# Kernel tuning notes

Hardware: AMD Instinct MI355X
Metric: run time of the kernel (lower is better)

## Reference

```python
import jax, jax.numpy as jnp
import numpy as np

B, N, CIN, H, D, K = 8, 1000, 16, 64, 16, 3  # batch, nodes, in_dim, hidden, embed_dim, cheb_k
XIN = CIN + H  # GRU concat input dim


def setup_inputs() -> dict:
    key = jax.random.key(0)
    ks = jax.random.split(key, 18)
    f = lambda k, s, sc=1.0: jax.random.normal(k, s, dtype=jnp.float32) * sc
    inp = {}
    inp['x1'] = f(ks[0], (B, N, CIN)); inp['x2'] = f(ks[1], (B, N, CIN)); inp['x3'] = f(ks[2], (B, N, CIN))
    inp['state1'] = f(ks[3], (B, N, H)); inp['state2'] = f(ks[4], (B, N, H)); inp['state3'] = f(ks[5], (B, N, H))
    for i, name in enumerate(['support1', 'support2', 'support3']):
        a = jax.random.uniform(ks[6 + i], (N, N), dtype=jnp.float32)
        inp[name] = a / a.sum(-1, keepdims=True)  # row-stochastic graph, keeps Chebyshev stable
    inp['embeddings1'] = f(ks[9], (N, D), 0.1); inp['embeddings2'] = f(ks[10], (N, D), 0.1); inp['embeddings3'] = f(ks[11], (N, D), 0.1)
    inp['mode_embedding'] = f(ks[12], (3, D), 0.5)
    # xavier-normal-ish scales for the hypernet weight pools
    inp['Wg'] = f(ks[13], (D, K * XIN, 2 * H), (2.0 / (K * XIN * 2 * H + D * 2 * H)) ** 0.5)
    inp['Bg'] = f(ks[14], (D, 2 * H), (2.0 / (D + 2 * H)) ** 0.5)
    inp['Wu'] = f(ks[15], (D, K * XIN, H), (2.0 / (K * XIN * H + D * H)) ** 0.5)
    inp['Bu'] = f(ks[16], (D, H), (2.0 / (D + H)) ** 0.5)
    return inp


def _cheb_gcn(x, support, emb, wp, bp):
    # x:[B,N,C], support:[N,N], emb:[N,D], wp:[D,K*C,O], bp:[D,O]
    # Chebyshev recurrence applied directly to features (equivalent to building T_k(support))
    terms = [x, jnp.einsum('nm,bmc->bnc', support, x)]
    for _ in range(2, K):
        terms.append(2.0 * jnp.einsum('nm,bmc->bnc', support, terms[-1]) - terms[-2])
    x_g = jnp.concatenate(terms, axis=-1)  # [B,N,K*C]
    # meta_axis='S': per-node weights = emb @ wp ; fused contraction
    out = jnp.einsum('bni,nd,dio->bno', x_g, emb, wp) + emb @ bp  # [B,N,O]
    return out


def _cell(x, state, support, emb, me, Wg, Bg, Wu, Bu):
    # me:[D] mode embedding scales the shared pools (einsum 'mc,cdf->mcdf' -> pick mode m)
    zr = jax.nn.sigmoid(_cheb_gcn(jnp.concatenate([x, state], -1), support, emb,
                                  me[:, None, None] * Wg, me[:, None] * Bg))
    z, r = jnp.split(zr, 2, axis=-1)
    hc = jnp.tanh(_cheb_gcn(jnp.concatenate([x, z * state], -1), support, emb,
                            me[:, None, None] * Wu, me[:, None] * Bu))
    return r * state + (1.0 - r) * hc


def reference(x1, x2, x3, state1, state2, state3, support1, support2, support3,
              embeddings1, embeddings2, embeddings3, mode_embedding, Wg, Bg, Wu, Bu):
    h1 = _cell(x1, state1, support1, embeddings1, mode_embedding[0], Wg, Bg, Wu, Bu)
    h2 = _cell(x2, state2, support2, embeddings2, mode_embedding[1], Wg, Bg, Wu, Bu)
    h3 = _cell(x3, state3, support3, embeddings3, mode_embedding[2], Wg, Bg, Wu, Bu)
    return (h1, h2, h3)
```

## Files before the change

kernel.cpp:

```cpp
#include <hip/hip_runtime.h>
#include <math.h>


typedef __attribute__((ext_vector_type(8))) short s16x8;
typedef __attribute__((ext_vector_type(4))) float f32x4;
typedef unsigned short u16;
typedef unsigned int u32;
typedef unsigned long long u64;

__device__ __forceinline__ u32 f2bf(float f) {
  union { float f; u32 u; } v; v.f = f;
  return (v.u + 0x7FFFu + ((v.u >> 16) & 1u)) >> 16;
}
__device__ __forceinline__ float bf2f(u16 h) {
  union { u32 u; float f; } v; v.u = (u32)h << 16; return v.f;
}
__device__ __forceinline__ void glds16(const u16* g, u16* l) {
  __builtin_amdgcn_global_load_lds(
      (const __attribute__((address_space(1))) void*)g,
      (__attribute__((address_space(3))) void*)l, 16, 0, 0);
}

#define E0 3145728
#define E1 1966080
#define E2 1920000
#define E3 384000
#define E4 384000
#define E5 384000
#define E6 119808

struct PrepArgs {
  const float* x[3]; const float* st[3]; const float* S[3];
  u16 *S16, *Xt, *Ag, *AgU, *T1t, *ZSt, *SZ1t;
};

__global__ void prep(PrepArgs P) {
  long idx = (long)blockIdx.x * 256 + threadIdx.x;
  if (idx < E0) {
    int m = (int)(idx >> 20); int rem = (int)(idx & 1048575);
    int n = rem >> 10, k = rem & 1023;
    float v = (n < 1000 && k < 1000) ? P.S[m][n * 1000 + k] : 0.f;
    P.S16[(size_t)m * 1048576 + rem] = (u16)f2bf(v); return;
  }
  idx -= E0;
  if (idx < E1) {
    int m = (int)(idx / 655360); int rem = (int)(idx % 655360);
    int col = rem >> 10, nn = rem & 1023;
    int b = col / 80, c = col % 80;
    float v = 0.f;
    if (nn < 1000) v = (c < 16) ? P.x[m][(b * 1000 + nn) * 16 + c]
                                : P.st[m][(b * 1000 + nn) * 64 + c - 16];
    P.Xt[(size_t)m * 655360 + rem] = (u16)f2bf(v); return;
  }
  idx -= E1;
  if (idx < E2) {
    int m = (int)(idx / 640000); int rem = (int)(idx % 640000);
    int r = rem / 80, c = rem % 80;
    int n = r >> 3, b = r & 7;
    float v = (c < 16) ? P.x[m][(b * 1000 + n) * 16 + c]
                       : P.st[m][(b * 1000 + n) * 64 + c - 16];
    P.Ag[(size_t)m * 2048000 + (size_t)r * 256 + c] = (u16)f2bf(v); return;
  }
  idx -= E2;
  if (idx < E3) {
    int m = (int)(idx / 128000); int rem = (int)(idx % 128000);
    int r = rem / 16, c = 240 + rem % 16;
    P.Ag[(size_t)m * 2048000 + (size_t)r * 256 + c] = 0; return;
  }
  idx -= E3;
  if (idx < E4) {
    int m = (int)(idx / 128000); int rem = (int)(idx % 128000);
    int r = rem / 16, c = rem % 16;
    int n = r >> 3, b = r & 7;
    P.AgU[(size_t)m * 2048000 + (size_t)r * 256 + c] =
        (u16)f2bf(P.x[m][(b * 1000 + n) * 16 + c]); return;
  }
  idx -= E4;
  if (idx < E5) {
    int m = (int)(idx / 128000); int rem = (int)(idx % 128000);
    int r = rem / 16, c = 240 + rem % 16;
    P.AgU[(size_t)m * 2048000 + (size_t)r * 256 + c] = 0; return;
  }
  idx -= E5;
  if (idx < E6) {
    int m = (int)(idx / 39936); int rem = (int)(idx % 39936);
    if (rem < 15360) { int col = rem / 24, j = rem % 24;
      P.T1t[(size_t)m * 655360 + col * 1024 + 1000 + j] = 0; }
    else if (rem < 27648) { int e = rem - 15360; int col = e / 24, j = e % 24;
      P.ZSt[(size_t)m * 524288 + col * 1024 + 1000 + j] = 0; }
    else { int e = rem - 27648; int col = e / 24, j = e % 24;
      P.SZ1t[(size_t)m * 524288 + col * 1024 + 1000 + j] = 0; }
    return;
  }
}

__global__ void bias_kernel(const float* __restrict__ e0, const float* __restrict__ e1,
                            const float* __restrict__ e2, const float* __restrict__ me,
                            const float* __restrict__ Bp, int O, float* __restrict__ outB) {
  int idx = blockIdx.x * blockDim.x + threadIdx.x;
  int total = 3 * 1000 * O;
  if (idx >= total) return;
  int mode = idx / (1000 * O);
  int rem  = idx % (1000 * O);
  int n = rem / O, o = rem % O;
  const float* emb = (mode == 0) ? e0 : (mode == 1) ? e1 : e2;
  float s = 0.f;
#pragma unroll
  for (int d = 0; d < 16; ++d)
    s += emb[n * 16 + d] * me[mode * 16 + d] * Bp[d * O + o];
  outB[idx] = s;
}

__global__ void packW_kernel(const float* __restrict__ Wg, const float* __restrict__ Wu,
                             u16* __restrict__ BtG, u16* __restrict__ BtU) {
  int idx = blockIdx.x * blockDim.x + threadIdx.x;
  if (idx >= (2048 + 1024) * 256) return;
  if (idx < 2048 * 256) {
    int col = idx >> 8, k = idx & 255;
    int d = col >> 7, o = col & 127;
    BtG[idx] = (k < 240) ? (u16)f2bf(Wg[d * 30720 + k * 128 + o]) : (u16)0;
  } else {
    int i2 = idx - 2048 * 256;
    int col = i2 >> 8, k = i2 & 255;
    int d = col >> 6, o = col & 63;
    BtU[i2] = (k < 240) ? (u16)f2bf(Wu[d * 15360 + k * 64 + o]) : (u16)0;
  }
}

struct ChebArgs2 {
  const u16* S16[3]; const u16* A[3]; const u16* Res[3];
  u16* Yt[3]; u16* AgA[3]; u16* AgX[3];
};

__global__ __launch_bounds__(256, 2) void cheb_v4(ChebArgs2 g, int fdiv, int agbase,
                                                  float alpha, float beta, int flags) {
  const int mode = blockIdx.z;
  const u16* __restrict__ Ab = g.A[mode];
  const u16* __restrict__ Sb = g.S16[mode];

  __shared__ u16 As[64 * 64];
  __shared__ u16 Bs[64 * 64];

  const int t = threadIdx.x;
  const int row0 = blockIdx.y * 64, n0 = blockIdx.x * 64;
  const int lane = t & 63, wid = t >> 6;
  const int l16 = lane & 15, quad = lane >> 4;
  const int wy = (wid >> 1) * 32, wx = (wid & 1) * 32;

  f32x4 acc[2][2];
#pragma unroll
  for (int a = 0; a < 2; ++a)
#pragma unroll
    for (int b = 0; b < 2; ++b) acc[a][b] = (f32x4){0.f, 0.f, 0.f, 0.f};

  for (int k0 = 0; k0 < 1024; k0 += 64) {
#pragma unroll
    for (int p = 0; p < 2; ++p) {
      int idx = p * 256 + t; int row = idx >> 3; int cs = (idx & 7) ^ (row & 7);
      glds16(Ab + (size_t)(row0 + row) * 1024 + k0 + cs * 8, &As[idx * 8]);
    }
#pragma unroll
    for (int p = 0; p < 2; ++p) {
      int idx = p * 256 + t; int row = idx >> 3; int cs = (idx & 7) ^ (row & 7);
      glds16(Sb + (size_t)(n0 + row) * 1024 + k0 + cs * 8, &Bs[idx * 8]);
    }
    __syncthreads();
    s16x8 af[2][2], bf[2][2];
#pragma unroll
    for (int mi = 0; mi < 2; ++mi) {
      int row = wy + mi * 16 + l16;
#pragma unroll
      for (int ks = 0; ks < 2; ++ks) {
        int cl = (ks * 4 + quad) ^ (row & 7);
        af[mi][ks] = *(const s16x8*)&As[row * 64 + cl * 8];
      }
    }
#pragma unroll
    for (int ni = 0; ni < 2; ++ni) {
      int row = wx + ni * 16 + l16;
#pragma unroll
      for (int ks = 0; ks < 2; ++ks) {
        int cl = (ks * 4 + quad) ^ (row & 7);
        bf[ni][ks] = *(const s16x8*)&Bs[row * 64 + cl * 8];
      }
    }
#pragma unroll
    for (int ks = 0; ks < 2; ++ks)
#pragma unroll
      for (int mi = 0; mi < 2; ++mi)
#pragma unroll
        for (int ni = 0; ni < 2; ++ni)
          acc[mi][ni] = __builtin_amdgcn_mfma_f32_16x16x32_bf16(af[mi][ks], bf[ni][ks], acc[mi][ni], 0, 0, 0);
    __syncthreads();
  }

#pragma unroll
  for (int mi = 0; mi < 2; ++mi) {
    int frow0 = row0 + wy + mi * 16 + quad * 4;
    int b = frow0 / fdiv, c0 = frow0 - b * fdiv;
#pragma unroll
    for (int ni = 0; ni < 2; ++ni) {
      int n = n0 + wx + ni * 16 + l16;
      if (n < 1000) {
        u16 pk[4];
#pragma unroll
        for (int r = 0; r < 4; ++r) {
          float v = alpha * acc[mi][ni][r];
          if (flags & 1) v += beta * bf2f(g.Res[mode][(size_t)(frow0 + r) * 1024 + n]);
          u16 h = (u16)f2bf(v);
          pk[r] = h;
          if (flags & 2) g.Yt[mode][(size_t)(frow0 + r) * 1024 + n] = h;
        }
        u64 pv = (u64)pk[0] | ((u64)pk[1] << 16) | ((u64)pk[2] << 32) | ((u64)pk[3] << 48);
        *(u64*)&g.AgA[mode][(size_t)(n * 8 + b) * 256 + agbase + c0] = pv;
        if ((flags & 4) && c0 < 16)
          *(u64*)&g.AgX[mode][(size_t)(n * 8 + b) * 256 + agbase + c0] = pv;
      }
    }
  }
}

struct Meta3Args {
  const u16* Ag;
  const u16* Bt;
  const float* emb[3];
  const float* me;
  const float* Bias;
  const float* state[3];
  u16* ZSt;
  u16* AgU;
  float* Rb;
  float* out;
};

__global__ __launch_bounds__(256, 4) void meta3(Meta3Args A, int is_gate, int O) {
  const int mode = blockIdx.z;
  const int row0 = blockIdx.y * 64;
  const int n0 = row0 >> 3;
  const int oc = blockIdx.x;
  const int ocbase = oc * 64;

  __shared__ u16 Bs[64 * 256];
  __shared__ float ewS[8][17];

  const int t = threadIdx.x;
  if (t < 128) {
    int nl = t >> 4, d = t & 15;
    ewS[nl][d] = A.emb[mode][(n0 + nl) * 16 + d] * A.me[mode * 16 + d];
  }

  const int lane = t & 63, wid = t >> 6;
  const int l16 = lane & 15, quad = lane >> 4;
  const int wy = (wid >> 1) * 32, wx = (wid & 1) * 32;
  const u16* Agm = A.Ag + (size_t)mode * 2048000;

#pragma unroll
  for (int p = 0; p < 8; ++p) {
    int idx = p * 256 + t; int row = idx >> 5; int cs = (idx & 31) ^ (row & 7);
    glds16(Agm + (size_t)(row0 + row) * 256 + cs * 8, &Bs[idx * 8]);
  }
  __syncthreads();

  s16x8 afr[2][8];
#pragma unroll
  for (int mi = 0; mi < 2; ++mi) {
    int row = wy + mi * 16 + l16;
#pragma unroll
    for (int ki = 0; ki < 8; ++ki) {
      int cl = (ki * 4 + quad) ^ (row & 7);
      afr[mi][ki] = *(const s16x8*)&Bs[row * 256 + cl * 8];
    }
  }
  __syncthreads();

  f32x4 outacc[2][2];
#pragma unroll
  for (int a = 0; a < 2; ++a)
#pragma unroll
    for (int b = 0; b < 2; ++b) outacc[a][b] = (f32x4){0.f, 0.f, 0.f, 0.f};

  for (int tl = 0; tl < 16; ++tl) {
    const int brow0 = tl * O + ocbase;
#pragma unroll
    for (int p = 0; p < 8; ++p) {
      int idx = p * 256 + t; int row = idx >> 5; int cs = (idx & 31) ^ (row & 7);
      glds16(A.Bt + (size_t)(brow0 + row) * 256 + cs * 8, &Bs[idx * 8]);
    }
    __syncthreads();

    f32x4 acc[2][2];
#pragma unroll
    for (int a = 0; a < 2; ++a)
#pragma unroll
      for (int b = 0; b < 2; ++b) acc[a][b] = (f32x4){0.f, 0.f, 0.f, 0.f};

#pragma unroll
    for (int ki = 0; ki < 8; ++ki) {
      s16x8 bfr[2];
#pragma unroll
      for (int ni = 0; ni < 2; ++ni) {
        int row = wx + ni * 16 + l16;
        int cl = (ki * 4 + quad) ^ (row & 7);
        bfr[ni] = *(const s16x8*)&Bs[row * 256 + cl * 8];
      }
#pragma unroll
      for (int mi = 0; mi < 2; ++mi)
#pragma unroll
        for (int ni = 0; ni < 2; ++ni)
          acc[mi][ni] = __builtin_amdgcn_mfma_f32_16x16x32_bf16(afr[mi][ki], bfr[ni], acc[mi][ni], 0, 0, 0);
    }

#pragma unroll
    for (int mi = 0; mi < 2; ++mi) {
      int nl = (wy + mi * 16 + quad * 4) >> 3;
      float s = ewS[nl][tl];
#pragma unroll
      for (int ni = 0; ni < 2; ++ni)
#pragma unroll
        for (int r = 0; r < 4; ++r)
          outacc[mi][ni][r] += s * acc[mi][ni][r];
    }
    __syncthreads();
  }

#pragma unroll
  for (int mi = 0; mi < 2; ++mi)
#pragma unroll
    for (int ni = 0; ni < 2; ++ni)
#pragma unroll
      for (int r = 0; r < 4; ++r) {
        int row = row0 + wy + mi * 16 + quad * 4 + r;
        int n = row >> 3, b = row & 7;
        int o = ocbase + wx + ni * 16 + l16;
        float pre = outacc[mi][ni][r] + A.Bias[(size_t)mode * 1000 * O + n * O + o];
        if (is_gate) {
          float sg = 1.f / (1.f + __expf(-pre));
          if (o < 64) {
            float st = A.state[mode][(b * 1000 + n) * 64 + o];
            float zs = sg * st;
            A.ZSt[(size_t)mode * 524288 + (size_t)(b * 64 + o) * 1024 + n] = (u16)f2bf(zs);
            A.AgU[(size_t)mode * 2048000 + (size_t)row * 256 + 16 + o] = (u16)f2bf(zs);
          } else {
            A.Rb[(size_t)mode * 512000 + row * 64 + (o - 64)] = sg;
          }
        } else {
          float hc = tanhf(pre);
          float rr = A.Rb[(size_t)mode * 512000 + row * 64 + o];
          float st = A.state[mode][(b * 1000 + n) * 64 + o];
          A.out[(size_t)mode * 512000 + (b * 1000 + n) * 64 + o] = rr * st + (1.f - rr) * hc;
        }
      }
}

extern "C" void kernel_launch(void* const* d_in, const int* in_sizes, int n_in,
                              void* d_out, int out_size, void* d_ws, size_t ws_size,
                              hipStream_t stream) {
  const float* x[3]   = {(const float*)d_in[0], (const float*)d_in[1], (const float*)d_in[2]};
  const float* st[3]  = {(const float*)d_in[3], (const float*)d_in[4], (const float*)d_in[5]};
  const float* S[3]   = {(const float*)d_in[6], (const float*)d_in[7], (const float*)d_in[8]};
  const float* emb[3] = {(const float*)d_in[9], (const float*)d_in[10], (const float*)d_in[11]};
  const float* me = (const float*)d_in[12];
  const float* Wg = (const float*)d_in[13];
  const float* Bg = (const float*)d_in[14];
  const float* Wu = (const float*)d_in[15];
  const float* Bu = (const float*)d_in[16];
  float* out = (float*)d_out;

  float* BiG = (float*)d_ws;
  float* BiU = BiG + 384000;
  float* Rb  = BiU + 192000;
  u16* S16 = (u16*)(Rb + 1536000);
  u16* Xt  = S16 + 3145728;
  u16* T1t = Xt + 1966080;
  u16* ZSt = T1t + 1966080;
  u16* SZ1t= ZSt + 1572864;
  u16* Ag  = SZ1t + 1572864;
  u16* AgU = Ag + 6144000;
  u16* BtG = AgU + 6144000;
  u16* BtU = BtG + 524288;

  {
    PrepArgs P;
    for (int m = 0; m < 3; ++m) { P.x[m] = x[m]; P.st[m] = st[m]; P.S[m] = S[m]; }
    P.S16 = S16; P.Xt = Xt; P.Ag = Ag; P.AgU = AgU; P.T1t = T1t; P.ZSt = ZSt; P.SZ1t = SZ1t;
    prep<<<32436, 256, 0, stream>>>(P);
  }
  bias_kernel<<<1500, 256, 0, stream>>>(emb[0], emb[1], emb[2], me, Bg, 128, BiG);
  bias_kernel<<<750, 256, 0, stream>>>(emb[0], emb[1], emb[2], me, Bu, 64, BiU);
  packW_kernel<<<3072, 256, 0, stream>>>(Wg, Wu, BtG, BtU);

  {
    ChebArgs2 a;
    for (int m = 0; m < 3; ++m) {
      a.S16[m] = S16 + (size_t)m * 1048576; a.A[m] = Xt + (size_t)m * 655360;
      a.Res[m] = nullptr; a.Yt[m] = T1t + (size_t)m * 655360;
      a.AgA[m] = Ag + (size_t)m * 2048000; a.AgX[m] = AgU + (size_t)m * 2048000;
    }
    cheb_v4<<<dim3(16, 10, 3), 256, 0, stream>>>(a, 80, 80, 1.f, 0.f, 2 | 4);
  }
  {
    ChebArgs2 a;
    for (int m = 0; m < 3; ++m) {
      a.S16[m] = S16 + (size_t)m * 1048576; a.A[m] = T1t + (size_t)m * 655360;
      a.Res[m] = Xt + (size_t)m * 655360; a.Yt[m] = nullptr;
      a.AgA[m] = Ag + (size_t)m * 2048000; a.AgX[m] = AgU + (size_t)m * 2048000;
    }
    cheb_v4<<<dim3(16, 10, 3), 256, 0, stream>>>(a, 80, 160, 2.f, -1.f, 1 | 4);
  }
  {
    Meta3Args a;
    a.Ag = Ag; a.Bt = BtG; a.me = me; a.Bias = BiG;
    a.ZSt = ZSt; a.AgU = AgU; a.Rb = Rb; a.out = out;
    for (int m = 0; m < 3; ++m) { a.emb[m] = emb[m]; a.state[m] = st[m]; }
    meta3<<<dim3(2, 125, 3), 256, 0, stream>>>(a, 1, 128);
  }
  {
    ChebArgs2 a;
    for (int m = 0; m < 3; ++m) {
      a.S16[m] = S16 + (size_t)m * 1048576; a.A[m] = ZSt + (size_t)m * 524288;
      a.Res[m] = nullptr; a.Yt[m] = SZ1t + (size_t)m * 524288;
      a.AgA[m] = AgU + (size_t)m * 2048000; a.AgX[m] = nullptr;
    }
    cheb_v4<<<dim3(16, 8, 3), 256, 0, stream>>>(a, 64, 96, 1.f, 0.f, 2);
  }
  {
    ChebArgs2 a;
    for (int m = 0; m < 3; ++m) {
      a.S16[m] = S16 + (size_t)m * 1048576; a.A[m] = SZ1t + (size_t)m * 524288;
      a.Res[m] = ZSt + (size_t)m * 524288; a.Yt[m] = nullptr;
      a.AgA[m] = AgU + (size_t)m * 2048000; a.AgX[m] = nullptr;
    }
    cheb_v4<<<dim3(16, 8, 3), 256, 0, stream>>>(a, 64, 176, 2.f, -1.f, 1);
  }
  {
    Meta3Args a;
    a.Ag = AgU; a.Bt = BtU; a.me = me; a.Bias = BiU;
    a.ZSt = ZSt; a.AgU = AgU; a.Rb = Rb; a.out = out;
    for (int m = 0; m < 3; ++m) { a.emb[m] = emb[m]; a.state[m] = st[m]; }
    meta3<<<dim3(1, 125, 3), 256, 0, stream>>>(a, 0, 64);
  }
}
```

Measured before the change: 271.7 us.

## Pre-swizzle weight pool into MFMA fragment layout and load B fragments directly

The weight-pool packing now writes bf16 weights in the exact per-lane MFMA B-fragment order, so meta3 can read B fragments straight from global memory into registers with coalesced 16-byte loads. This removes the per-tile LDS staging of B and the two block-wide barriers per tile. The price is more register pressure from holding 16 fragment vectors, so launch bounds drop from 4 to 3 blocks per SM, and every wave now issues its own global loads (likely L2-served) where the block used to share one LDS copy.

New measurement: 280.3 us. 1.03x slower.

```diff
diff --git a/kernel.cpp b/kernel.cpp
--- a/kernel.cpp
+++ b/kernel.cpp
@@ -115,14 +115,18 @@
                              u16* __restrict__ BtG, u16* __restrict__ BtU) {
   int idx = blockIdx.x * blockDim.x + threadIdx.x;
   if (idx >= (2048 + 1024) * 256) return;
-  if (idx < 2048 * 256) {
-    int col = idx >> 8, k = idx & 255;
-    int d = col >> 7, o = col & 127;
+  if (idx < 524288) {
+    int e = idx & 7, lane = (idx >> 3) & 63, ki = (idx >> 9) & 7;
+    int j = (idx >> 12) & 7, d = idx >> 15;
+    int k = ki * 32 + (lane >> 4) * 8 + e;
+    int o = j * 16 + (lane & 15);
     BtG[idx] = (k < 240) ? (u16)f2bf(Wg[d * 30720 + k * 128 + o]) : (u16)0;
   } else {
-    int i2 = idx - 2048 * 256;
-    int col = i2 >> 8, k = i2 & 255;
-    int d = col >> 6, o = col & 63;
+    int i2 = idx - 524288;
+    int e = i2 & 7, lane = (i2 >> 3) & 63, ki = (i2 >> 9) & 7;
+    int j = (i2 >> 12) & 3, d = i2 >> 14;
+    int k = ki * 32 + (lane >> 4) * 8 + e;
+    int o = j * 16 + (lane & 15);
     BtU[i2] = (k < 240) ? (u16)f2bf(Wu[d * 15360 + k * 64 + o]) : (u16)0;
   }
 }
@@ -233,14 +237,15 @@
   float* out;
 };
 
-__global__ __launch_bounds__(256, 4) void meta3(Meta3Args A, int is_gate, int O) {
+__global__ __launch_bounds__(256, 3) void meta3(Meta3Args A, int is_gate, int O) {
   const int mode = blockIdx.z;
   const int row0 = blockIdx.y * 64;
   const int n0 = row0 >> 3;
   const int oc = blockIdx.x;
   const int ocbase = oc * 64;
-
-  __shared__ u16 Bs[64 * 256];
+  const int J = O >> 4;
+
+  __shared__ u16 As[64 * 256];
   __shared__ float ewS[8][17];
 
   const int t = threadIdx.x;
@@ -257,7 +262,7 @@
 #pragma unroll
   for (int p = 0; p < 8; ++p) {
     int idx = p * 256 + t; int row = idx >> 5; int cs = (idx & 31) ^ (row & 7);
-    glds16(Agm + (size_t)(row0 + row) * 256 + cs * 8, &Bs[idx * 8]);
+    glds16(Agm + (size_t)(row0 + row) * 256 + cs * 8, &As[idx * 8]);
   }
   __syncthreads();
 
@@ -268,10 +273,9 @@
 #pragma unroll
     for (int ki = 0; ki < 8; ++ki) {
       int cl = (ki * 4 + quad) ^ (row & 7);
-      afr[mi][ki] = *(const s16x8*)&Bs[row * 256 + cl * 8];
-    }
-  }
-  __syncthreads();
+      afr[mi][ki] = *(const s16x8*)&As[row * 256 + cl * 8];
+    }
+  }
 
   f32x4 outacc[2][2];
 #pragma unroll
@@ -279,14 +283,16 @@
 #pragma unroll
     for (int b = 0; b < 2; ++b) outacc[a][b] = (f32x4){0.f, 0.f, 0.f, 0.f};
 
+  const s16x8* __restrict__ Bf = (const s16x8*)A.Bt;
+  const int jb = oc * 4 + (wx >> 4);
+
   for (int tl = 0; tl < 16; ++tl) {
-    const int brow0 = tl * O + ocbase;
-#pragma unroll
-    for (int p = 0; p < 8; ++p) {
-      int idx = p * 256 + t; int row = idx >> 5; int cs = (idx & 31) ^ (row & 7);
-      glds16(A.Bt + (size_t)(brow0 + row) * 256 + cs * 8, &Bs[idx * 8]);
-    }
-    __syncthreads();
+    s16x8 bfr[2][8];
+#pragma unroll
+    for (int ni = 0; ni < 2; ++ni)
+#pragma unroll
+      for (int ki = 0; ki < 8; ++ki)
+        bfr[ni][ki] = Bf[(((tl * J + jb + ni) * 8 + ki) << 6) + lane];
 
     f32x4 acc[2][2];
 #pragma unroll
@@ -295,20 +301,12 @@
       for (int b = 0; b < 2; ++b) acc[a][b] = (f32x4){0.f, 0.f, 0.f, 0.f};
 
 #pragma unroll
-    for (int ki = 0; ki < 8; ++ki) {
-      s16x8 bfr[2];
-#pragma unroll
-      for (int ni = 0; ni < 2; ++ni) {
-        int row = wx + ni * 16 + l16;
-        int cl = (ki * 4 + quad) ^ (row & 7);
-        bfr[ni] = *(const s16x8*)&Bs[row * 256 + cl * 8];
-      }
+    for (int ki = 0; ki < 8; ++ki)
 #pragma unroll
       for (int mi = 0; mi < 2; ++mi)
 #pragma unroll
         for (int ni = 0; ni < 2; ++ni)
-          acc[mi][ni] = __builtin_amdgcn_mfma_f32_16x16x32_bf16(afr[mi][ki], bfr[ni], acc[mi][ni], 0, 0, 0);
-    }
+          acc[mi][ni] = __builtin_amdgcn_mfma_f32_16x16x32_bf16(afr[mi][ki], bfr[ni][ki], acc[mi][ni], 0, 0, 0);
 
 #pragma unroll
     for (int mi = 0; mi < 2; ++mi) {
@@ -320,7 +318,6 @@
         for (int r = 0; r < 4; ++r)
           outacc[mi][ni][r] += s * acc[mi][ni][r];
     }
-    __syncthreads();
   }
 
 #pragma unroll
```

## Double-buffer weight tiles in meta3 with half-K stages and async prefetch

Applied to the files above, without the earlier changes.

The meta3 kernel used to load each 64x256 weight tile into a single LDS buffer and synchronize before and after every tile, so global loads never overlapped MFMA work. It now splits each tile into two 128-wide halves held in a two-slot LDS ring. The load for stage hs+2 is issued while stage hs computes, using explicit vmcnt/lgkmcnt waits and raw barriers in place of __syncthreads. LDS use stays the same, but correctness now depends on the hand-written wait counts matching the number of outstanding global_load_lds ops per stage.

Result: slower. 409.5 us (+50.7%).

```diff
diff --git a/kernel.cpp b/kernel.cpp
--- a/kernel.cpp
+++ b/kernel.cpp
@@ -240,7 +240,7 @@
   const int oc = blockIdx.x;
   const int ocbase = oc * 64;
 
-  __shared__ u16 Bs[64 * 256];
+  __shared__ u16 Bs[2][64 * 128];
   __shared__ float ewS[8][17];
 
   const int t = threadIdx.x;
@@ -253,13 +253,15 @@
   const int l16 = lane & 15, quad = lane >> 4;
   const int wy = (wid >> 1) * 32, wx = (wid & 1) * 32;
   const u16* Agm = A.Ag + (size_t)mode * 2048000;
+  u16* Asf = &Bs[0][0];
 
 #pragma unroll
   for (int p = 0; p < 8; ++p) {
     int idx = p * 256 + t; int row = idx >> 5; int cs = (idx & 31) ^ (row & 7);
-    glds16(Agm + (size_t)(row0 + row) * 256 + cs * 8, &Bs[idx * 8]);
-  }
-  __syncthreads();
+    glds16(Agm + (size_t)(row0 + row) * 256 + cs * 8, &Asf[idx * 8]);
+  }
+  asm volatile("s_waitcnt vmcnt(0)" ::: "memory");
+  __builtin_amdgcn_s_barrier();
 
   s16x8 afr[2][8];
 #pragma unroll
@@ -268,60 +270,82 @@
 #pragma unroll
     for (int ki = 0; ki < 8; ++ki) {
       int cl = (ki * 4 + quad) ^ (row & 7);
-      afr[mi][ki] = *(const s16x8*)&Bs[row * 256 + cl * 8];
-    }
-  }
-  __syncthreads();
-
-  f32x4 outacc[2][2];
+      afr[mi][ki] = *(const s16x8*)&Asf[row * 256 + cl * 8];
+    }
+  }
+  asm volatile("s_waitcnt lgkmcnt(0)" ::: "memory");
+  __builtin_amdgcn_s_barrier();
+
+#define STAGE_H(HS)                                                         \
+  {                                                                         \
+    int d_ = (HS) >> 1, k0_ = ((HS) & 1) << 7;                              \
+    const u16* src_ = A.Bt + (size_t)(d_ * O + ocbase) * 256 + k0_;         \
+    u16* dst_ = &Bs[(HS) & 1][0];                                           \
+    _Pragma("unroll")                                                       \
+    for (int p_ = 0; p_ < 4; ++p_) {                                        \
+      int idx_ = p_ * 256 + t; int row_ = idx_ >> 4;                        \
+      int cs_ = (idx_ & 15) ^ (row_ & 7);                                   \
+      glds16(src_ + (size_t)row_ * 256 + cs_ * 8, dst_ + idx_ * 8);         \
+    }                                                                       \
+  }
+
+  STAGE_H(0);
+  STAGE_H(1);
+
+  f32x4 outacc[2][2], acc[2][2];
 #pragma unroll
   for (int a = 0; a < 2; ++a)
 #pragma unroll
-    for (int b = 0; b < 2; ++b) outacc[a][b] = (f32x4){0.f, 0.f, 0.f, 0.f};
-
-  for (int tl = 0; tl < 16; ++tl) {
-    const int brow0 = tl * O + ocbase;
-#pragma unroll
-    for (int p = 0; p < 8; ++p) {
-      int idx = p * 256 + t; int row = idx >> 5; int cs = (idx & 31) ^ (row & 7);
-      glds16(A.Bt + (size_t)(brow0 + row) * 256 + cs * 8, &Bs[idx * 8]);
-    }
-    __syncthreads();
-
-    f32x4 acc[2][2];
-#pragma unroll
-    for (int a = 0; a < 2; ++a)
-#pragma unroll
-      for (int b = 0; b < 2; ++b) acc[a][b] = (f32x4){0.f, 0.f, 0.f, 0.f};
-
-#pragma unroll
-    for (int ki = 0; ki < 8; ++ki) {
+    for (int b = 0; b < 2; ++b) {
+      outacc[a][b] = (f32x4){0.f, 0.f, 0.f, 0.f};
+      acc[a][b] = (f32x4){0.f, 0.f, 0.f, 0.f};
+    }
+
+  for (int hs = 0; hs < 32; ++hs) {
+    if (hs < 31) asm volatile("s_waitcnt vmcnt(4)" ::: "memory");
+    else         asm volatile("s_waitcnt vmcnt(0)" ::: "memory");
+    __builtin_amdgcn_s_barrier();
+
+    const u16* buf = &Bs[hs & 1][0];
+    const int kbase = (hs & 1) << 2;
+#pragma unroll
+    for (int kil = 0; kil < 4; ++kil) {
       s16x8 bfr[2];
 #pragma unroll
       for (int ni = 0; ni < 2; ++ni) {
         int row = wx + ni * 16 + l16;
-        int cl = (ki * 4 + quad) ^ (row & 7);
-        bfr[ni] = *(const s16x8*)&Bs[row * 256 + cl * 8];
+        int cl = (kil * 4 + quad) ^ (row & 7);
+        bfr[ni] = *(const s16x8*)&buf[row * 128 + cl * 8];
       }
 #pragma unroll
       for (int mi = 0; mi < 2; ++mi)
 #pragma unroll
         for (int ni = 0; ni < 2; ++ni)
-          acc[mi][ni] = __builtin_amdgcn_mfma_f32_16x16x32_bf16(afr[mi][ki], bfr[ni], acc[mi][ni], 0, 0, 0);
-    }
-
-#pragma unroll
-    for (int mi = 0; mi < 2; ++mi) {
-      int nl = (wy + mi * 16 + quad * 4) >> 3;
-      float s = ewS[nl][tl];
-#pragma unroll
-      for (int ni = 0; ni < 2; ++ni)
-#pragma unroll
-        for (int r = 0; r < 4; ++r)
-          outacc[mi][ni][r] += s * acc[mi][ni][r];
-    }
-    __syncthreads();
-  }
+          acc[mi][ni] = __builtin_amdgcn_mfma_f32_16x16x32_bf16(
+              afr[mi][kbase + kil], bfr[ni], acc[mi][ni], 0, 0, 0);
+    }
+
+    if (hs & 1) {
+      int d = hs >> 1;
+#pragma unroll
+      for (int mi = 0; mi < 2; ++mi) {
+        int nl = (wy + mi * 16 + quad * 4) >> 3;
+        float s = ewS[nl][d];
+#pragma unroll
+        for (int ni = 0; ni < 2; ++ni) {
+#pragma unroll
+          for (int r = 0; r < 4; ++r)
+            outacc[mi][ni][r] += s * acc[mi][ni][r];
+          acc[mi][ni] = (f32x4){0.f, 0.f, 0.f, 0.f};
+        }
+      }
+    }
+
+    asm volatile("s_waitcnt lgkmcnt(0)" ::: "memory");
+    __builtin_amdgcn_s_barrier();
+    if (hs + 2 < 32) STAGE_H(hs + 2);
+  }
+#undef STAGE_H
 
 #pragma unroll
   for (int mi = 0; mi < 2; ++mi)
```
